# Kernel tuning notes

Hardware: AMD Instinct MI355X
Metric: run time of the kernel (lower is better)

Reference implementation:

```python
import jax, jax.numpy as jnp
import numpy as np

N = 50000   # num_nodes
E = 640000  # num_edges (avg degree ~12.8)
D = 128     # input_dim
H = 128     # hidden_dim
T = 100     # targets per head


def setup_inputs() -> dict:
    key = jax.random.key(0)
    ks = jax.random.split(key, 20)
    w = lambda k, s: jax.random.normal(k, s, jnp.float32) * 0.02
    return {
        "x": jax.random.normal(ks[0], (N, D), jnp.float32),
        "edge_index": jax.random.randint(ks[1], (2, E), 0, N, dtype=jnp.int32),
        "edge_weight": jax.random.uniform(ks[2], (E,), jnp.float32),
        "ace_idx": jax.random.randint(ks[3], (T,), 0, N, dtype=jnp.int32),
        "h2_idx": jax.random.randint(ks[4], (T,), 0, N, dtype=jnp.int32),
        "W1": w(ks[5], (D, H)), "b1": jnp.zeros((H,), jnp.float32),
        "W2": w(ks[6], (H, H)), "b2": jnp.zeros((H,), jnp.float32),
        "W3": w(ks[7], (H, H)), "b3": jnp.zeros((H,), jnp.float32),
        "Wh": w(ks[8], (H, H)), "bh": jnp.zeros((H,), jnp.float32),
        "Wace": w(ks[9], (H, 1)), "bace": jnp.zeros((1,), jnp.float32),
        "Wh2": w(ks[10], (H, 1)), "bh2": jnp.zeros((1,), jnp.float32),
    }


def gcn_conv(x, src, dst, ew, W, b):
    # PyG GCNConv: add self-loops (weight 1), symmetric D^-1/2 (A+I) D^-1/2, then XW + b
    n = x.shape[0]
    xw = x @ W                                             # [N, H]
    deg = jax.ops.segment_sum(ew, dst, num_segments=n) + 1.0  # +1 from self-loop
    dinv = jax.lax.rsqrt(jnp.maximum(deg, 1e-12))          # deg >= 1 here
    norm = dinv[src] * ew * dinv[dst]                      # per-edge coefficient
    agg = jax.ops.segment_sum(norm[:, None] * xw[src], dst, num_segments=n)
    agg = agg + (dinv * dinv)[:, None] * xw                # self-loop contribution
    return agg + b


def reference(x, edge_index, edge_weight, ace_idx, h2_idx,
              W1, b1, W2, b2, W3, b3, Wh, bh, Wace, bace, Wh2, bh2):
    src, dst = edge_index[0], edge_index[1]
    h = jax.nn.relu(gcn_conv(x, src, dst, edge_weight, W1, b1))
    h = jax.nn.relu(gcn_conv(h, src, dst, edge_weight, W2, b2))
    h = jax.nn.relu(gcn_conv(h, src, dst, edge_weight, W3, b3))
    # dropout is identity in eval mode
    h = jax.nn.relu(h @ Wh + bh)
    ace_pred = h[ace_idx] @ Wace + bace   # [T, 1]
    h2_pred = h[h2_idx] @ Wh2 + bh2       # [T, 1]
    return jnp.concatenate([ace_pred, h2_pred], axis=0)  # [2T, 1]
```

## Files before the change

kernel.cpp:

```cpp
#include <hip/hip_runtime.h>
#include <math.h>

constexpr int N = 50000;
constexpr int E = 640000;
constexpr int D = 128;
constexpr int T = 100;
constexpr int NB = (N + 255) / 256;
constexpr int MAXDEG = 64;
constexpr float SC = 256.0f;
constexpr float SCINV = 1.0f / 256.0f;

typedef __attribute__((ext_vector_type(8))) _Float16 half8v;
typedef __attribute__((ext_vector_type(8))) unsigned short ushort8v;
typedef __attribute__((ext_vector_type(4))) float f32x4;


__global__ void edge_pass_kernel(const float* __restrict__ ew, const int* __restrict__ src,
                                 const int* __restrict__ dst,
                                 unsigned long long* __restrict__ degcnt,
                                 unsigned int* __restrict__ slot) {
  int e = blockIdx.x * 256 + threadIdx.x;
  if (e < E) {
    float w = ew[e];
    int d = dst[e];
    unsigned int fxdeg = __float2uint_rn(w * 16777216.0f);
    unsigned int fx16 = __float2uint_rn(w * 65536.0f);
    if (fx16 > 65535u) fx16 = 65535u;
    unsigned long long old = atomicAdd(&degcnt[d],
                                       ((unsigned long long)fxdeg << 32) | 1ull);
    unsigned int rank = (unsigned int)(old & 0xffffffffull);
    if (rank < MAXDEG)
      slot[(size_t)d * MAXDEG + rank] = (fx16 << 16) | (unsigned int)src[e];
  }
}


__global__ __launch_bounds__(256) void prep_kernel(
    const uint2* __restrict__ degcnt, float* __restrict__ dinv,
    const float* __restrict__ W0, const float* __restrict__ W1,
    const float* __restrict__ W2, unsigned short* __restrict__ wt,
    unsigned short* __restrict__ w3kn) {
  if (blockIdx.x < NB) {
    int i = blockIdx.x * 256 + threadIdx.x;
    if (i < N) {
      uint2 p = degcnt[i];
      float d = (float)p.y * (1.0f / 16777216.0f) + 1.0f;
      dinv[i] = 1.0f / sqrtf(d);
    }
  } else {
    int idx = (blockIdx.x - NB) * 256 + threadIdx.x;
    int layer = idx >> 14;
    int r = idx & 16383;
    int k = r & 127, n = r >> 7;
    const float* W = layer == 0 ? W0 : layer == 1 ? W1 : W2;
    float v = W[k * D + n] * (layer == 0 ? SC : 1.0f);
    _Float16 h = (_Float16)v;
    unsigned short bits = *(unsigned short*)&h;
    wt[layer * 16384 + n * D + k] = bits;
    if (layer == 2) w3kn[k * D + n] = bits;
  }
}


__device__ inline void stage_B(const unsigned short* __restrict__ Wt,
                               unsigned short* __restrict__ Bl, int tid) {
  constexpr int SB = 136;
#pragma unroll
  for (int it = 0; it < 8; ++it) {
    int idx = tid + it * 256;
    int r = idx >> 4;
    int c8 = idx & 15;
    ushort8v v = *(const ushort8v*)&Wt[r * D + c8 * 8];
    *(ushort8v*)&Bl[r * SB + c8 * 8] = v;
  }
}

__device__ inline void mfma_core_and_store(
    const unsigned short* __restrict__ Bl, half8v (*a)[2], const float* __restrict__ dinv,
    int row0, int rbase, int q, int n16, unsigned short* __restrict__ out) {
  constexpr int SB = 136;
  f32x4 acc[2][8] = {};
#pragma unroll
  for (int kc = 0; kc < 4; ++kc) {
    const int ko = kc * 32 + q * 8;
#pragma unroll
    for (int ct = 0; ct < 8; ++ct) {
      int n = ct * 16 + n16;
      half8v b = *(const half8v*)&Bl[n * SB + ko];
#pragma unroll
      for (int rt = 0; rt < 2; ++rt) {
        acc[rt][ct] = __builtin_amdgcn_mfma_f32_16x16x32_f16(a[kc][rt], b, acc[rt][ct], 0, 0, 0);
      }
    }
  }
#pragma unroll
  for (int rt = 0; rt < 2; ++rt) {
#pragma unroll
    for (int r = 0; r < 4; ++r) {
      int gr = row0 + rbase + rt * 16 + q * 4 + r;
      if (gr < N) {
        float dv = dinv[gr];
#pragma unroll
        for (int ct = 0; ct < 8; ++ct) {
          int col = ct * 16 + n16;
          _Float16 h = (_Float16)(acc[rt][ct][r] * dv);
          out[(size_t)gr * D + col] = *(unsigned short*)&h;
        }
      }
    }
  }
}

__global__ __launch_bounds__(256) void gemm_mfma_kernel(
    const unsigned short* __restrict__ A, const unsigned short* __restrict__ Wt,
    const float* __restrict__ dinv, unsigned short* __restrict__ out) {
  constexpr int SB = 136;
  __shared__ unsigned short Bl[128 * SB];
  const int tid = threadIdx.x;
  const int row0 = blockIdx.x * 128;
  stage_B(Wt, Bl, tid);
  __syncthreads();

  const int w = tid >> 6, lane = tid & 63;
  const int q = lane >> 4, n16 = lane & 15;
  const int rbase = w * 32;
  size_t arow[2];
#pragma unroll
  for (int rt = 0; rt < 2; ++rt) {
    int gr = row0 + rbase + rt * 16 + n16;
    if (gr >= N) gr = N - 1;
    arow[rt] = (size_t)gr * D;
  }
  half8v a[4][2];
#pragma unroll
  for (int kc = 0; kc < 4; ++kc) {
    const int ko = kc * 32 + q * 8;
#pragma unroll
    for (int rt = 0; rt < 2; ++rt)
      a[kc][rt] = *(const half8v*)&A[arow[rt] + ko];
  }
  mfma_core_and_store(Bl, a, dinv, row0, rbase, q, n16, out);
}

__global__ __launch_bounds__(256) void gemm_mfma_f32_kernel(
    const float* __restrict__ A, const unsigned short* __restrict__ Wt,
    const float* __restrict__ dinv, unsigned short* __restrict__ out) {
  constexpr int SB = 136;
  __shared__ unsigned short Bl[128 * SB];
  const int tid = threadIdx.x;
  const int row0 = blockIdx.x * 128;
  stage_B(Wt, Bl, tid);
  __syncthreads();

  const int w = tid >> 6, lane = tid & 63;
  const int q = lane >> 4, n16 = lane & 15;
  const int rbase = w * 32;
  size_t arow[2];
#pragma unroll
  for (int rt = 0; rt < 2; ++rt) {
    int gr = row0 + rbase + rt * 16 + n16;
    if (gr >= N) gr = N - 1;
    arow[rt] = (size_t)gr * D;
  }
  half8v a[4][2];
#pragma unroll
  for (int kc = 0; kc < 4; ++kc) {
    const int ko = kc * 32 + q * 8;
#pragma unroll
    for (int rt = 0; rt < 2; ++rt) {
      float4 v0 = *(const float4*)&A[arow[rt] + ko];
      float4 v1 = *(const float4*)&A[arow[rt] + ko + 4];
      half8v h;
      h[0] = (_Float16)v0.x; h[1] = (_Float16)v0.y;
      h[2] = (_Float16)v0.z; h[3] = (_Float16)v0.w;
      h[4] = (_Float16)v1.x; h[5] = (_Float16)v1.y;
      h[6] = (_Float16)v1.z; h[7] = (_Float16)v1.w;
      a[kc][rt] = h;
    }
  }
  mfma_core_and_store(Bl, a, dinv, row0, rbase, q, n16, out);
}


__global__ __launch_bounds__(256) void agg_kernel(
    const unsigned short* __restrict__ z, const unsigned int* __restrict__ slot,
    const uint2* __restrict__ degcnt, const float* __restrict__ dinv,
    const float* __restrict__ bias, unsigned short* __restrict__ oP) {
  int g = (blockIdx.x * 256 + threadIdx.x) >> 4;
  int lane = threadIdx.x & 15;

  int cnt = (int)degcnt[g].x; if (cnt > MAXDEG) cnt = MAXDEG;
  half8v xv = *(const half8v*)&z[(size_t)g * D + lane * 8];
  float acc[8];
#pragma unroll
  for (int i = 0; i < 8; ++i) acc[i] = (float)xv[i];

  const unsigned int* sl = slot + (size_t)g * MAXDEG;
  int k = 0;
  for (; k + 4 <= cnt; k += 4) {
    uint4 p = *(const uint4*)&sl[k];
    float c0 = (float)(p.x >> 16) * (1.0f / 65536.0f);
    float c1 = (float)(p.y >> 16) * (1.0f / 65536.0f);
    float c2 = (float)(p.z >> 16) * (1.0f / 65536.0f);
    float c3 = (float)(p.w >> 16) * (1.0f / 65536.0f);
    half8v v0 = *(const half8v*)&z[(size_t)(p.x & 0xffffu) * D + lane * 8];
    half8v v1 = *(const half8v*)&z[(size_t)(p.y & 0xffffu) * D + lane * 8];
    half8v v2 = *(const half8v*)&z[(size_t)(p.z & 0xffffu) * D + lane * 8];
    half8v v3 = *(const half8v*)&z[(size_t)(p.w & 0xffffu) * D + lane * 8];
#pragma unroll
    for (int i = 0; i < 8; ++i) {
      acc[i] = fmaf(c0, (float)v0[i], acc[i]);
      acc[i] = fmaf(c1, (float)v1[i], acc[i]);
      acc[i] = fmaf(c2, (float)v2[i], acc[i]);
      acc[i] = fmaf(c3, (float)v3[i], acc[i]);
    }
  }
  for (; k < cnt; ++k) {
    unsigned int p = sl[k];
    float c = (float)(p >> 16) * (1.0f / 65536.0f);
    half8v v = *(const half8v*)&z[(size_t)(p & 0xffffu) * D + lane * 8];
#pragma unroll
    for (int i = 0; i < 8; ++i) acc[i] = fmaf(c, (float)v[i], acc[i]);
  }

  float dv = dinv[g];
  half8v hv;
#pragma unroll
  for (int i = 0; i < 8; ++i)
    hv[i] = (_Float16)fmaxf(fmaf(dv, acc[i], bias[lane * 8 + i] * SC), 0.f);
  *(half8v*)&oP[(size_t)g * D + lane * 8] = hv;
}


__global__ __launch_bounds__(256) void l23_heads_kernel(
    const unsigned short* __restrict__ z2, const unsigned int* __restrict__ slot,
    const uint2* __restrict__ degcnt, const float* __restrict__ dinv,
    const float* __restrict__ b2, const float* __restrict__ b3,
    const unsigned short* __restrict__ w3kn,
    const float* __restrict__ Wh, const float* __restrict__ bh,
    const int* __restrict__ ace_idx, const int* __restrict__ h2_idx,
    const float* __restrict__ Wace, const float* __restrict__ bace,
    const float* __restrict__ Wh2, const float* __restrict__ bh2,
    float* __restrict__ out) {
  __shared__ float sacc[16][128];
  __shared__ unsigned short w3l[16384];
  __shared__ float svec[128];
  __shared__ float h3v[128];
  __shared__ float psum[2];
  int t = blockIdx.x;
  int tid = threadIdx.x;
  int node; const float* whead; float bhead;
  if (t < T) { node = ace_idx[t];     whead = Wace; bhead = bace[0]; }
  else       { node = h2_idx[t - T];  whead = Wh2;  bhead = bh2[0]; }

#pragma unroll
  for (int it = 0; it < 8; ++it) {
    int idx = tid + it * 256;
    *(ushort8v*)&w3l[idx * 8] = *(const ushort8v*)&w3kn[idx * 8];
  }

  int grp = tid >> 4, lane = tid & 15;
  float b2l[8];
#pragma unroll
  for (int i = 0; i < 8; ++i) b2l[i] = b2[lane * 8 + i] * SC;

  int tcnt = (int)degcnt[node].x; if (tcnt > MAXDEG) tcnt = MAXDEG;
  const unsigned int* tsl = slot + (size_t)node * MAXDEG;
  int nitems = 1 + tcnt;
  float a[8] = {};
  for (int it = grp; it < nitems; it += 16) {
    int u; float wgt;
    if (it == 0) { u = node; wgt = 1.0f; }
    else {
      unsigned int p = tsl[it - 1];
      wgt = (float)(p >> 16) * (1.0f / 65536.0f);
      u = (int)(p & 0xffffu);
    }
    float dvu = dinv[u];
    half8v xv = *(const half8v*)&z2[(size_t)u * D + lane * 8];
    float r[8];
#pragma unroll
    for (int i = 0; i < 8; ++i) r[i] = (float)xv[i];
    int cu = (int)degcnt[u].x; if (cu > MAXDEG) cu = MAXDEG;
    const unsigned int* usl = slot + (size_t)u * MAXDEG;
    int e = 0;
    for (; e + 4 <= cu; e += 4) {
      uint4 p4 = *(const uint4*)&usl[e];
      float c0 = (float)(p4.x >> 16) * (1.0f / 65536.0f);
      float c1 = (float)(p4.y >> 16) * (1.0f / 65536.0f);
      float c2 = (float)(p4.z >> 16) * (1.0f / 65536.0f);
      float c3 = (float)(p4.w >> 16) * (1.0f / 65536.0f);
      half8v v0 = *(const half8v*)&z2[(size_t)(p4.x & 0xffffu) * D + lane * 8];
      half8v v1 = *(const half8v*)&z2[(size_t)(p4.y & 0xffffu) * D + lane * 8];
      half8v v2 = *(const half8v*)&z2[(size_t)(p4.z & 0xffffu) * D + lane * 8];
      half8v v3 = *(const half8v*)&z2[(size_t)(p4.w & 0xffffu) * D + lane * 8];
#pragma unroll
      for (int i = 0; i < 8; ++i) {
        r[i] = fmaf(c0, (float)v0[i], r[i]);
        r[i] = fmaf(c1, (float)v1[i], r[i]);
        r[i] = fmaf(c2, (float)v2[i], r[i]);
        r[i] = fmaf(c3, (float)v3[i], r[i]);
      }
    }
    for (; e < cu; ++e) {
      unsigned int p2 = usl[e];
      float c2 = (float)(p2 >> 16) * (1.0f / 65536.0f);
      half8v v = *(const half8v*)&z2[(size_t)(p2 & 0xffffu) * D + lane * 8];
#pragma unroll
      for (int i = 0; i < 8; ++i) r[i] = fmaf(c2, (float)v[i], r[i]);
    }
#pragma unroll
    for (int i = 0; i < 8; ++i) {
      float h2 = fmaxf(fmaf(dvu, r[i], b2l[i]), 0.f);
      a[i] = fmaf(wgt, dvu * h2, a[i]);
    }
  }
#pragma unroll
  for (int i = 0; i < 8; ++i) sacc[grp][lane * 8 + i] = a[i];
  __syncthreads();

  if (tid < 128) {
    float s = 0.f;
#pragma unroll
    for (int gp = 0; gp < 16; ++gp) s += sacc[gp][tid];
    svec[tid] = s * dinv[node];
  }
  __syncthreads();

  if (tid < 128) {
    float y = b3[tid] * SC;
#pragma unroll 16
    for (int k = 0; k < 128; ++k) {
      _Float16 wv = *(const _Float16*)&w3l[k * D + tid];
      y = fmaf(svec[k], (float)wv, y);
    }
    h3v[tid] = fmaxf(y, 0.f) * SCINV;
  }
  __syncthreads();

  float v = 0.f;
  if (tid < 128) {
    float acc = bh[tid];
#pragma unroll 16
    for (int k = 0; k < 128; ++k)
      acc = fmaf(h3v[k], Wh[k * D + tid], acc);
    v = fmaxf(acc, 0.f) * whead[tid];
  }
#pragma unroll
  for (int off = 32; off; off >>= 1) v += __shfl_down(v, off, 64);
  if (tid < 128 && (tid & 63) == 0) psum[tid >> 6] = v;
  __syncthreads();
  if (tid == 0) out[t] = psum[0] + psum[1] + bhead;
}


extern "C" void kernel_launch(void* const* d_in, const int* in_sizes, int n_in,
                              void* d_out, int out_size, void* d_ws, size_t ws_size,
                              hipStream_t stream) {
  const float* x    = (const float*)d_in[0];
  const int*   ei   = (const int*)d_in[1];
  const float* ew   = (const float*)d_in[2];
  const int*   ace  = (const int*)d_in[3];
  const int*   h2   = (const int*)d_in[4];
  const float* W1 = (const float*)d_in[5];  const float* b1 = (const float*)d_in[6];
  const float* W2 = (const float*)d_in[7];  const float* b2 = (const float*)d_in[8];
  const float* W3 = (const float*)d_in[9];  const float* b3 = (const float*)d_in[10];
  const float* Wh = (const float*)d_in[11]; const float* bh = (const float*)d_in[12];
  const float* Wace = (const float*)d_in[13]; const float* bace = (const float*)d_in[14];
  const float* Wh2  = (const float*)d_in[15]; const float* bh2  = (const float*)d_in[16];
  const int* src = ei;
  const int* dst = ei + E;

  char* w = (char*)d_ws;
  unsigned long long* degcnt = (unsigned long long*)w;  w += (size_t)N * 8;
  float* dinv   = (float*)w;              w += N * 4;
  unsigned int* slot = (unsigned int*)w;  w += (size_t)N * MAXDEG * 4;
  unsigned short* wt = (unsigned short*)w; w += 3 * 16384 * 2;
  unsigned short* w3kn = (unsigned short*)w; w += 16384 * 2;
  unsigned short* zbuf = (unsigned short*)w; w += (size_t)N * D * 2;
  unsigned short* P1  = (unsigned short*)w; w += (size_t)N * D * 2;

  hipMemsetAsync(degcnt, 0, (size_t)N * 8, stream);
  edge_pass_kernel<<<(E + 255) / 256, 256, 0, stream>>>(ew, src, dst, degcnt, slot);
  prep_kernel<<<NB + 192, 256, 0, stream>>>((const uint2*)degcnt, dinv, W1, W2, W3, wt, w3kn);

  const int GB = (N + 127) / 128;
  const int AG = N * 16 / 256;

  gemm_mfma_f32_kernel<<<GB, 256, 0, stream>>>(x, wt + 0 * 16384, dinv, zbuf);
  agg_kernel<<<AG, 256, 0, stream>>>(zbuf, slot, (const uint2*)degcnt, dinv, b1, P1);
  gemm_mfma_kernel<<<GB, 256, 0, stream>>>(P1, wt + 1 * 16384, dinv, zbuf);
  l23_heads_kernel<<<2 * T, 256, 0, stream>>>(zbuf, slot, (const uint2*)degcnt, dinv,
                                              b2, b3, w3kn, Wh, bh, ace, h2,
                                              Wace, bace, Wh2, bh2, (float*)d_out);
}
```

Before: 214.1 us.

## Fuse edge pass, weight prep and first GEMM into one launch; compute dinv on the fly

Merges the edge-scatter kernel, weight conversion kernel and first-layer GEMM into a single block-partitioned launch. This works because layer-1 XW no longer applies the source-side dinv; the aggregation applies dinv per neighbour instead, recomputed from the degree word. The dinv buffer and its prep pass are removed, and the sqrt is recomputed wherever it is needed. This cuts two launches and their serial dependency in exchange for an extra gathered degree read and a reciprocal sqrt per edge in the aggregation.

Measured after the change: 207.1 us. 1.03x faster.

```diff
diff --git a/kernel.cpp b/kernel.cpp
--- a/kernel.cpp
+++ b/kernel.cpp
@@ -5,59 +5,147 @@
 constexpr int E = 640000;
 constexpr int D = 128;
 constexpr int T = 100;
-constexpr int NB = (N + 255) / 256;
 constexpr int MAXDEG = 64;
 constexpr float SC = 256.0f;
 constexpr float SCINV = 1.0f / 256.0f;
+constexpr int GB = (N + 127) / 128;
+constexpr int EB = (E + 255) / 256;
+constexpr int WB = 2 * 16384 / 256;
 
 typedef __attribute__((ext_vector_type(8))) _Float16 half8v;
 typedef __attribute__((ext_vector_type(8))) unsigned short ushort8v;
 typedef __attribute__((ext_vector_type(4))) float f32x4;
 
-
-__global__ void edge_pass_kernel(const float* __restrict__ ew, const int* __restrict__ src,
-                                 const int* __restrict__ dst,
-                                 unsigned long long* __restrict__ degcnt,
-                                 unsigned int* __restrict__ slot) {
-  int e = blockIdx.x * 256 + threadIdx.x;
-  if (e < E) {
-    float w = ew[e];
-    int d = dst[e];
-    unsigned int fxdeg = __float2uint_rn(w * 16777216.0f);
-    unsigned int fx16 = __float2uint_rn(w * 65536.0f);
-    if (fx16 > 65535u) fx16 = 65535u;
-    unsigned long long old = atomicAdd(&degcnt[d],
-                                       ((unsigned long long)fxdeg << 32) | 1ull);
-    unsigned int rank = (unsigned int)(old & 0xffffffffull);
-    if (rank < MAXDEG)
-      slot[(size_t)d * MAXDEG + rank] = (fx16 << 16) | (unsigned int)src[e];
-  }
-}
-
-
-__global__ __launch_bounds__(256) void prep_kernel(
-    const uint2* __restrict__ degcnt, float* __restrict__ dinv,
-    const float* __restrict__ W0, const float* __restrict__ W1,
-    const float* __restrict__ W2, unsigned short* __restrict__ wt,
-    unsigned short* __restrict__ w3kn) {
-  if (blockIdx.x < NB) {
-    int i = blockIdx.x * 256 + threadIdx.x;
-    if (i < N) {
-      uint2 p = degcnt[i];
-      float d = (float)p.y * (1.0f / 16777216.0f) + 1.0f;
-      dinv[i] = 1.0f / sqrtf(d);
+__device__ inline float dinv_of(unsigned int degY) {
+  return 1.0f / sqrtf((float)degY * (1.0f / 16777216.0f) + 1.0f);
+}
+
+
+template <bool DINV>
+__device__ inline void mfma_core_and_store(
+    const unsigned short* __restrict__ Bl, half8v (*a)[2],
+    const uint2* __restrict__ degcnt,
+    int row0, int rbase, int q, int n16, unsigned short* __restrict__ out) {
+  constexpr int SB = 136;
+  f32x4 acc[2][8] = {};
+#pragma unroll
+  for (int kc = 0; kc < 4; ++kc) {
+    const int ko = kc * 32 + q * 8;
+#pragma unroll
+    for (int ct = 0; ct < 8; ++ct) {
+      int n = ct * 16 + n16;
+      half8v b = *(const half8v*)&Bl[n * SB + ko];
+#pragma unroll
+      for (int rt = 0; rt < 2; ++rt) {
+        acc[rt][ct] = __builtin_amdgcn_mfma_f32_16x16x32_f16(a[kc][rt], b, acc[rt][ct], 0, 0, 0);
+      }
+    }
+  }
+#pragma unroll
+  for (int rt = 0; rt < 2; ++rt) {
+#pragma unroll
+    for (int r = 0; r < 4; ++r) {
+      int gr = row0 + rbase + rt * 16 + q * 4 + r;
+      if (gr < N) {
+        float dv = 1.0f;
+        if (DINV) dv = dinv_of(degcnt[gr].y);
+#pragma unroll
+        for (int ct = 0; ct < 8; ++ct) {
+          int col = ct * 16 + n16;
+          _Float16 h = (_Float16)(DINV ? acc[rt][ct][r] * dv : acc[rt][ct][r]);
+          out[(size_t)gr * D + col] = *(unsigned short*)&h;
+        }
+      }
+    }
+  }
+}
+
+
+__global__ __launch_bounds__(256) void fused_build_kernel(
+    const float* __restrict__ x, const float* __restrict__ W1,
+    const float* __restrict__ W2, const float* __restrict__ W3,
+    const float* __restrict__ ew, const int* __restrict__ src,
+    const int* __restrict__ dst,
+    unsigned long long* __restrict__ degcnt, unsigned int* __restrict__ slot,
+    unsigned short* __restrict__ wt1, unsigned short* __restrict__ w3kn,
+    unsigned short* __restrict__ z1) {
+  constexpr int SB = 136;
+  __shared__ unsigned short Bl[128 * SB];
+  const int b = blockIdx.x;
+  const int tid = threadIdx.x;
+
+  if (b < GB) {
+#pragma unroll
+    for (int it = 0; it < 16; ++it) {
+      int idx4 = tid + it * 256;
+      int e = idx4 * 4;
+      int k = e >> 7, n = e & 127;
+      float4 v = *(const float4*)&W1[e];
+      _Float16 h0 = (_Float16)(v.x * SC);
+      _Float16 h1 = (_Float16)(v.y * SC);
+      _Float16 h2 = (_Float16)(v.z * SC);
+      _Float16 h3 = (_Float16)(v.w * SC);
+      Bl[(n + 0) * SB + k] = *(unsigned short*)&h0;
+      Bl[(n + 1) * SB + k] = *(unsigned short*)&h1;
+      Bl[(n + 2) * SB + k] = *(unsigned short*)&h2;
+      Bl[(n + 3) * SB + k] = *(unsigned short*)&h3;
+    }
+    __syncthreads();
+
+    const int w = tid >> 6, lane = tid & 63;
+    const int q = lane >> 4, n16 = lane & 15;
+    const int rbase = w * 32;
+    const int row0 = b * 128;
+    size_t arow[2];
+#pragma unroll
+    for (int rt = 0; rt < 2; ++rt) {
+      int gr = row0 + rbase + rt * 16 + n16;
+      if (gr >= N) gr = N - 1;
+      arow[rt] = (size_t)gr * D;
+    }
+    half8v a[4][2];
+#pragma unroll
+    for (int kc = 0; kc < 4; ++kc) {
+      const int ko = kc * 32 + q * 8;
+#pragma unroll
+      for (int rt = 0; rt < 2; ++rt) {
+        float4 v0 = *(const float4*)&x[arow[rt] + ko];
+        float4 v1 = *(const float4*)&x[arow[rt] + ko + 4];
+        half8v h;
+        h[0] = (_Float16)v0.x; h[1] = (_Float16)v0.y;
+        h[2] = (_Float16)v0.z; h[3] = (_Float16)v0.w;
+        h[4] = (_Float16)v1.x; h[5] = (_Float16)v1.y;
+        h[6] = (_Float16)v1.z; h[7] = (_Float16)v1.w;
+        a[kc][rt] = h;
+      }
+    }
+    mfma_core_and_store<false>(Bl, a, nullptr, row0, rbase, q, n16, z1);
+  } else if (b < GB + EB) {
+    int e = (b - GB) * 256 + tid;
+    if (e < E) {
+      float w = ew[e];
+      int d = dst[e];
+      unsigned int fxdeg = __float2uint_rn(w * 16777216.0f);
+      unsigned int fx16 = __float2uint_rn(w * 65536.0f);
+      if (fx16 > 65535u) fx16 = 65535u;
+      unsigned long long old = atomicAdd(&degcnt[d],
+                                         ((unsigned long long)fxdeg << 32) | 1ull);
+      unsigned int rank = (unsigned int)(old & 0xffffffffull);
+      if (rank < MAXDEG)
+        slot[(size_t)d * MAXDEG + rank] = (fx16 << 16) | (unsigned int)src[e];
     }
   } else {
-    int idx = (blockIdx.x - NB) * 256 + threadIdx.x;
+    int idx = (b - GB - EB) * 256 + tid;
     int layer = idx >> 14;
     int r = idx & 16383;
     int k = r & 127, n = r >> 7;
-    const float* W = layer == 0 ? W0 : layer == 1 ? W1 : W2;
-    float v = W[k * D + n] * (layer == 0 ? SC : 1.0f);
-    _Float16 h = (_Float16)v;
-    unsigned short bits = *(unsigned short*)&h;
-    wt[layer * 16384 + n * D + k] = bits;
-    if (layer == 2) w3kn[k * D + n] = bits;
+    if (layer == 0) {
+      _Float16 h = (_Float16)W2[k * D + n];
+      wt1[n * D + k] = *(unsigned short*)&h;
+    } else {
+      _Float16 h = (_Float16)W3[k * D + n];
+      w3kn[k * D + n] = *(unsigned short*)&h;
+    }
   }
 }
 
@@ -75,45 +163,9 @@
   }
 }
 
-__device__ inline void mfma_core_and_store(
-    const unsigned short* __restrict__ Bl, half8v (*a)[2], const float* __restrict__ dinv,
-    int row0, int rbase, int q, int n16, unsigned short* __restrict__ out) {
-  constexpr int SB = 136;
-  f32x4 acc[2][8] = {};
-#pragma unroll
-  for (int kc = 0; kc < 4; ++kc) {
-    const int ko = kc * 32 + q * 8;
-#pragma unroll
-    for (int ct = 0; ct < 8; ++ct) {
-      int n = ct * 16 + n16;
-      half8v b = *(const half8v*)&Bl[n * SB + ko];
-#pragma unroll
-      for (int rt = 0; rt < 2; ++rt) {
-        acc[rt][ct] = __builtin_amdgcn_mfma_f32_16x16x32_f16(a[kc][rt], b, acc[rt][ct], 0, 0, 0);
-      }
-    }
-  }
-#pragma unroll
-  for (int rt = 0; rt < 2; ++rt) {
-#pragma unroll
-    for (int r = 0; r < 4; ++r) {
-      int gr = row0 + rbase + rt * 16 + q * 4 + r;
-      if (gr < N) {
-        float dv = dinv[gr];
-#pragma unroll
-        for (int ct = 0; ct < 8; ++ct) {
-          int col = ct * 16 + n16;
-          _Float16 h = (_Float16)(acc[rt][ct][r] * dv);
-          out[(size_t)gr * D + col] = *(unsigned short*)&h;
-        }
-      }
-    }
-  }
-}
-
 __global__ __launch_bounds__(256) void gemm_mfma_kernel(
     const unsigned short* __restrict__ A, const unsigned short* __restrict__ Wt,
-    const float* __restrict__ dinv, unsigned short* __restrict__ out) {
+    const uint2* __restrict__ degcnt, unsigned short* __restrict__ out) {
   constexpr int SB = 136;
   __shared__ unsigned short Bl[128 * SB];
   const int tid = threadIdx.x;
@@ -139,70 +191,38 @@
     for (int rt = 0; rt < 2; ++rt)
       a[kc][rt] = *(const half8v*)&A[arow[rt] + ko];
   }
-  mfma_core_and_store(Bl, a, dinv, row0, rbase, q, n16, out);
-}
-
-__global__ __launch_bounds__(256) void gemm_mfma_f32_kernel(
-    const float* __restrict__ A, const unsigned short* __restrict__ Wt,
-    const float* __restrict__ dinv, unsigned short* __restrict__ out) {
-  constexpr int SB = 136;
-  __shared__ unsigned short Bl[128 * SB];
-  const int tid = threadIdx.x;
-  const int row0 = blockIdx.x * 128;
-  stage_B(Wt, Bl, tid);
-  __syncthreads();
-
-  const int w = tid >> 6, lane = tid & 63;
-  const int q = lane >> 4, n16 = lane & 15;
-  const int rbase = w * 32;
-  size_t arow[2];
-#pragma unroll
-  for (int rt = 0; rt < 2; ++rt) {
-    int gr = row0 + rbase + rt * 16 + n16;
-    if (gr >= N) gr = N - 1;
-    arow[rt] = (size_t)gr * D;
-  }
-  half8v a[4][2];
-#pragma unroll
-  for (int kc = 0; kc < 4; ++kc) {
-    const int ko = kc * 32 + q * 8;
-#pragma unroll
-    for (int rt = 0; rt < 2; ++rt) {
-      float4 v0 = *(const float4*)&A[arow[rt] + ko];
-      float4 v1 = *(const float4*)&A[arow[rt] + ko + 4];
-      half8v h;
-      h[0] = (_Float16)v0.x; h[1] = (_Float16)v0.y;
-      h[2] = (_Float16)v0.z; h[3] = (_Float16)v0.w;
-      h[4] = (_Float16)v1.x; h[5] = (_Float16)v1.y;
-      h[6] = (_Float16)v1.z; h[7] = (_Float16)v1.w;
-      a[kc][rt] = h;
-    }
-  }
-  mfma_core_and_store(Bl, a, dinv, row0, rbase, q, n16, out);
+  mfma_core_and_store<true>(Bl, a, degcnt, row0, rbase, q, n16, out);
 }
 
 
 __global__ __launch_bounds__(256) void agg_kernel(
     const unsigned short* __restrict__ z, const unsigned int* __restrict__ slot,
-    const uint2* __restrict__ degcnt, const float* __restrict__ dinv,
-    const float* __restrict__ bias, unsigned short* __restrict__ oP) {
+    const uint2* __restrict__ degcnt, const float* __restrict__ bias,
+    unsigned short* __restrict__ oP) {
   int g = (blockIdx.x * 256 + threadIdx.x) >> 4;
   int lane = threadIdx.x & 15;
-
-  int cnt = (int)degcnt[g].x; if (cnt > MAXDEG) cnt = MAXDEG;
+  const unsigned int* degY = (const unsigned int*)degcnt;
+
+  uint2 pg = degcnt[g];
+  int cnt = (int)pg.x; if (cnt > MAXDEG) cnt = MAXDEG;
+  float dvg = dinv_of(pg.y);
   half8v xv = *(const half8v*)&z[(size_t)g * D + lane * 8];
   float acc[8];
 #pragma unroll
-  for (int i = 0; i < 8; ++i) acc[i] = (float)xv[i];
+  for (int i = 0; i < 8; ++i) acc[i] = dvg * (float)xv[i];
 
   const unsigned int* sl = slot + (size_t)g * MAXDEG;
   int k = 0;
   for (; k + 4 <= cnt; k += 4) {
     uint4 p = *(const uint4*)&sl[k];
-    float c0 = (float)(p.x >> 16) * (1.0f / 65536.0f);
-    float c1 = (float)(p.y >> 16) * (1.0f / 65536.0f);
-    float c2 = (float)(p.z >> 16) * (1.0f / 65536.0f);
-    float c3 = (float)(p.w >> 16) * (1.0f / 65536.0f);
+    float d0 = dinv_of(degY[((p.x & 0xffffu) << 1) + 1]);
+    float d1 = dinv_of(degY[((p.y & 0xffffu) << 1) + 1]);
+    float d2 = dinv_of(degY[((p.z & 0xffffu) << 1) + 1]);
+    float d3 = dinv_of(degY[((p.w & 0xffffu) << 1) + 1]);
+    float c0 = (float)(p.x >> 16) * (1.0f / 65536.0f) * d0;
+    float c1 = (float)(p.y >> 16) * (1.0f / 65536.0f) * d1;
+    float c2 = (float)(p.z >> 16) * (1.0f / 65536.0f) * d2;
+    float c3 = (float)(p.w >> 16) * (1.0f / 65536.0f) * d3;
     half8v v0 = *(const half8v*)&z[(size_t)(p.x & 0xffffu) * D + lane * 8];
     half8v v1 = *(const half8v*)&z[(size_t)(p.y & 0xffffu) * D + lane * 8];
     half8v v2 = *(const half8v*)&z[(size_t)(p.z & 0xffffu) * D + lane * 8];
@@ -217,24 +237,24 @@
   }
   for (; k < cnt; ++k) {
     unsigned int p = sl[k];
-    float c = (float)(p >> 16) * (1.0f / 65536.0f);
+    float dsv = dinv_of(degY[((p & 0xffffu) << 1) + 1]);
+    float c = (float)(p >> 16) * (1.0f / 65536.0f) * dsv;
     half8v v = *(const half8v*)&z[(size_t)(p & 0xffffu) * D + lane * 8];
 #pragma unroll
     for (int i = 0; i < 8; ++i) acc[i] = fmaf(c, (float)v[i], acc[i]);
   }
 
-  float dv = dinv[g];
   half8v hv;
 #pragma unroll
   for (int i = 0; i < 8; ++i)
-    hv[i] = (_Float16)fmaxf(fmaf(dv, acc[i], bias[lane * 8 + i] * SC), 0.f);
+    hv[i] = (_Float16)fmaxf(fmaf(dvg, acc[i], bias[lane * 8 + i] * SC), 0.f);
   *(half8v*)&oP[(size_t)g * D + lane * 8] = hv;
 }
 
 
 __global__ __launch_bounds__(256) void l23_heads_kernel(
     const unsigned short* __restrict__ z2, const unsigned int* __restrict__ slot,
-    const uint2* __restrict__ degcnt, const float* __restrict__ dinv,
+    const uint2* __restrict__ degcnt,
     const float* __restrict__ b2, const float* __restrict__ b3,
     const unsigned short* __restrict__ w3kn,
     const float* __restrict__ Wh, const float* __restrict__ bh,
@@ -264,7 +284,9 @@
 #pragma unroll
   for (int i = 0; i < 8; ++i) b2l[i] = b2[lane * 8 + i] * SC;
 
-  int tcnt = (int)degcnt[node].x; if (tcnt > MAXDEG) tcnt = MAXDEG;
+  uint2 pn = degcnt[node];
+  int tcnt = (int)pn.x; if (tcnt > MAXDEG) tcnt = MAXDEG;
+  float dvn = dinv_of(pn.y);
   const unsigned int* tsl = slot + (size_t)node * MAXDEG;
   int nitems = 1 + tcnt;
   float a[8] = {};
@@ -276,12 +298,13 @@
       wgt = (float)(p >> 16) * (1.0f / 65536.0f);
       u = (int)(p & 0xffffu);
     }
-    float dvu = dinv[u];
+    uint2 pu = degcnt[u];
+    float dvu = dinv_of(pu.y);
+    int cu = (int)pu.x; if (cu > MAXDEG) cu = MAXDEG;
     half8v xv = *(const half8v*)&z2[(size_t)u * D + lane * 8];
     float r[8];
 #pragma unroll
     for (int i = 0; i < 8; ++i) r[i] = (float)xv[i];
-    int cu = (int)degcnt[u].x; if (cu > MAXDEG) cu = MAXDEG;
     const unsigned int* usl = slot + (size_t)u * MAXDEG;
     int e = 0;
     for (; e + 4 <= cu; e += 4) {
@@ -323,7 +346,7 @@
     float s = 0.f;
 #pragma unroll
     for (int gp = 0; gp < 16; ++gp) s += sacc[gp][tid];
-    svec[tid] = s * dinv[node];
+    svec[tid] = s * dvn;
   }
   __syncthreads();
 
@@ -373,24 +396,20 @@
 
   char* w = (char*)d_ws;
   unsigned long long* degcnt = (unsigned long long*)w;  w += (size_t)N * 8;
-  float* dinv   = (float*)w;              w += N * 4;
   unsigned int* slot = (unsigned int*)w;  w += (size_t)N * MAXDEG * 4;
-  unsigned short* wt = (unsigned short*)w; w += 3 * 16384 * 2;
+  unsigned short* wt1 = (unsigned short*)w;  w += 16384 * 2;
   unsigned short* w3kn = (unsigned short*)w; w += 16384 * 2;
   unsigned short* zbuf = (unsigned short*)w; w += (size_t)N * D * 2;
-  unsigned short* P1  = (unsigned short*)w; w += (size_t)N * D * 2;
+  unsigned short* P1  = (unsigned short*)w;  w += (size_t)N * D * 2;
+
+  const int AG = N * 16 / 256;
 
   hipMemsetAsync(degcnt, 0, (size_t)N * 8, stream);
-  edge_pass_kernel<<<(E + 255) / 256, 256, 0, stream>>>(ew, src, dst, degcnt, slot);
-  prep_kernel<<<NB + 192, 256, 0, stream>>>((const uint2*)degcnt, dinv, W1, W2, W3, wt, w3kn);
-
-  const int GB = (N + 127) / 128;
-  const int AG = N * 16 / 256;
-
-  gemm_mfma_f32_kernel<<<GB, 256, 0, stream>>>(x, wt + 0 * 16384, dinv, zbuf);
-  agg_kernel<<<AG, 256, 0, stream>>>(zbuf, slot, (const uint2*)degcnt, dinv, b1, P1);
-  gemm_mfma_kernel<<<GB, 256, 0, stream>>>(P1, wt + 1 * 16384, dinv, zbuf);
-  l23_heads_kernel<<<2 * T, 256, 0, stream>>>(zbuf, slot, (const uint2*)degcnt, dinv,
+  fused_build_kernel<<<GB + EB + WB, 256, 0, stream>>>(
+      x, W1, W2, W3, ew, src, dst, degcnt, slot, wt1, w3kn, zbuf);
+  agg_kernel<<<AG, 256, 0, stream>>>(zbuf, slot, (const uint2*)degcnt, b1, P1);
+  gemm_mfma_kernel<<<GB, 256, 0, stream>>>(P1, wt1, (const uint2*)degcnt, zbuf);
+  l23_heads_kernel<<<2 * T, 256, 0, stream>>>(zbuf, slot, (const uint2*)degcnt,
                                               b2, b3, w3kn, Wh, bh, ace, h2,
                                               Wace, bace, Wh2, bh2, (float*)d_out);
 }
```
